# Kernel tuning notes

Measured on AMD Instinct MI355X. Metric: run time of the kernel, lower is better.

Reference implementation:

```python
import jax, jax.numpy as jnp
import numpy as np

B, M, N, P, Q, GRID, DIM = 8, 64, 64, 3, 3, 512, 3


def _clamped_knots(n_ctrl, p):
    # clamped uniform knot vector of length n_ctrl + p + 1
    interior = np.linspace(0.0, 1.0, n_ctrl - p + 1)[1:-1]
    return np.concatenate([np.zeros(p + 1), interior, np.ones(p + 1)]).astype(np.float32)


def _find_span(u, knots, n_ctrl, p):
    spans = np.searchsorted(knots, u, side='right') - 1
    return np.clip(spans, p, n_ctrl - 1).astype(np.int32)


def _basis_funs(u, spans, knots, p):
    # Cox-de Boor (Algorithm A2.2, The NURBS Book), vectorized over the grid
    G = u.shape[0]
    Nb = np.zeros((G, p + 1), np.float32)
    Nb[:, 0] = 1.0
    left = np.zeros((G, p + 1), np.float32)
    right = np.zeros((G, p + 1), np.float32)
    for j in range(1, p + 1):
        left[:, j] = u - knots[spans + 1 - j]
        right[:, j] = knots[spans + j] - u
        saved = np.zeros(G, np.float32)
        for r in range(j):
            temp = Nb[:, r] / (right[:, r + 1] + left[:, j - r])
            Nb[:, r] = saved + right[:, r + 1] * temp
            saved = left[:, j - r] * temp
        Nb[:, j] = saved
    return Nb


def setup_inputs() -> dict:
    key = jax.random.key(0)
    k1, k2 = jax.random.split(key)
    U = _clamped_knots(M, P)
    V = _clamped_knots(N, Q)
    u = np.linspace(0.0, 1.0, GRID, dtype=np.float32)
    v = np.linspace(0.0, 1.0, GRID, dtype=np.float32)
    uspan = _find_span(u, U, M, P)
    vspan = _find_span(v, V, N, Q)
    Nu = _basis_funs(u, uspan, U, P)
    Nv = _basis_funs(v, vspan, V, Q)
    xyz = jax.random.normal(k1, (B, M, N, DIM), jnp.float32)
    w = jax.random.uniform(k2, (B, M, N, 1), jnp.float32, minval=0.5, maxval=1.5)
    ctrl_pts = jnp.concatenate([xyz * w, w], axis=-1)  # homogeneous [B,M,N,4]
    return {
        'ctrl_pts': ctrl_pts,
        'uspan': jnp.asarray(uspan),
        'vspan': jnp.asarray(vspan),
        'Nu': jnp.asarray(Nu),
        'Nv': jnp.asarray(Nv),
    }


def reference(ctrl_pts, uspan, vspan, Nu, Nv):
    # surfaces[b,i,j,:] = sum_{r,s} Nu[i,r] Nv[j,s] ctrl[b, uspan[i]-P+r, vspan[j]-Q+s, :]
    idx_u = uspan[:, None] - P + jnp.arange(P + 1)   # [G, P+1]
    idx_v = vspan[:, None] - Q + jnp.arange(Q + 1)   # [G, Q+1]
    pts_u = ctrl_pts[:, idx_u]                        # [B, G, P+1, N, 4] gather
    Su = jnp.einsum('gr,bgrnd->bgnd', Nu, pts_u)      # [B, G, N, 4]
    pts_v = Su[:, :, idx_v]                           # [B, G, G, Q+1, 4] gather
    Sw = jnp.einsum('hs,bghsd->bghd', Nv, pts_v)      # [B, G, G, 4] homogeneous
    return Sw[..., :DIM] / Sw[..., DIM:DIM + 1]       # perspective divide
```

## Files before the change

### kernel.cpp

```cpp
#include <hip/hip_runtime.h>

#define GRID_PTS 512
#define M_CTRL   64
#define N_CTRL   64

__global__ __launch_bounds__(128) void surfeval_kernel(
    const float4* __restrict__ ctrl,
    const int*    __restrict__ uspan,
    const int*    __restrict__ vspan,
    const float4* __restrict__ Nu,
    const float4* __restrict__ Nv,
    float*        __restrict__ out)
{
    __shared__ float4 Su[N_CTRL];

    const int blk = blockIdx.x;
    const int g   = blk & (GRID_PTS - 1);
    const int b   = blk >> 9;
    const int t   = threadIdx.x;

    if (t < N_CTRL) {
        const int    iu = uspan[g] - 3;
        const float4 nu = Nu[g];
        const float4* cp = ctrl + ((size_t)b * M_CTRL + iu) * N_CTRL + t;
        const float4 c0 = cp[0 * N_CTRL];
        const float4 c1 = cp[1 * N_CTRL];
        const float4 c2 = cp[2 * N_CTRL];
        const float4 c3 = cp[3 * N_CTRL];
        float4 s;
        s.x = nu.x * c0.x + nu.y * c1.x + nu.z * c2.x + nu.w * c3.x;
        s.y = nu.x * c0.y + nu.y * c1.y + nu.z * c2.y + nu.w * c3.y;
        s.z = nu.x * c0.z + nu.y * c1.z + nu.z * c2.z + nu.w * c3.z;
        s.w = nu.x * c0.w + nu.y * c1.w + nu.z * c2.w + nu.w * c3.w;
        Su[t] = s;
    }
    __syncthreads();

    const int h0 = t * 4;
    float r[12];
#pragma unroll
    for (int i = 0; i < 4; ++i) {
        const int    h  = h0 + i;
        const int    iv = vspan[h] - 3;
        const float4 nv = Nv[h];
        const float4 a0 = Su[iv + 0];
        const float4 a1 = Su[iv + 1];
        const float4 a2 = Su[iv + 2];
        const float4 a3 = Su[iv + 3];
        const float sx = nv.x * a0.x + nv.y * a1.x + nv.z * a2.x + nv.w * a3.x;
        const float sy = nv.x * a0.y + nv.y * a1.y + nv.z * a2.y + nv.w * a3.y;
        const float sz = nv.x * a0.z + nv.y * a1.z + nv.z * a2.z + nv.w * a3.z;
        const float sw = nv.x * a0.w + nv.y * a1.w + nv.z * a2.w + nv.w * a3.w;
        const float inv = 1.0f / sw;
        r[i * 3 + 0] = sx * inv;
        r[i * 3 + 1] = sy * inv;
        r[i * 3 + 2] = sz * inv;
    }

    float4* op = (float4*)(out + ((size_t)blk * GRID_PTS + h0) * 3);
    op[0] = make_float4(r[0], r[1], r[2],  r[3]);
    op[1] = make_float4(r[4], r[5], r[6],  r[7]);
    op[2] = make_float4(r[8], r[9], r[10], r[11]);
}

extern "C" void kernel_launch(void* const* d_in, const int* in_sizes, int n_in,
                              void* d_out, int out_size, void* d_ws, size_t ws_size,
                              hipStream_t stream) {
    const float4* ctrl  = (const float4*)d_in[0];
    const int*    uspan = (const int*)d_in[1];
    const int*    vspan = (const int*)d_in[2];
    const float4* Nu    = (const float4*)d_in[3];
    const float4* Nv    = (const float4*)d_in[4];
    float*        out   = (float*)d_out;

    const int blocks = 8 * GRID_PTS;
    surfeval_kernel<<<blocks, 128, 0, stream>>>(ctrl, uspan, vspan, Nu, Nv, out);
}
```

Baseline: 75.66 us.

## Hoist Nv/vspan loads before barrier, use fast rcp and nontemporal stores

Moves each thread's vspan and Nv loads ahead of the Su computation and barrier so their latency overlaps with the first stage. It replaces the IEEE division with the hardware reciprocal builtin and writes the output with nontemporal vector stores to avoid polluting cache. The output writes dominate traffic, so the nontemporal stores target write bandwidth. The fast reciprocal slightly reduces precision.

```diff
diff --git a/kernel.cpp b/kernel.cpp
--- a/kernel.cpp
+++ b/kernel.cpp
@@ -3,6 +3,8 @@
 #define GRID_PTS 512
 #define M_CTRL   64
 #define N_CTRL   64
+
+typedef float vfloat4 __attribute__((ext_vector_type(4)));
 
 __global__ __launch_bounds__(128) void surfeval_kernel(
     const float4* __restrict__ ctrl,
@@ -18,6 +20,15 @@
     const int g   = blk & (GRID_PTS - 1);
     const int b   = blk >> 9;
     const int t   = threadIdx.x;
+    const int h0  = t * 4;
+
+    int    iv[4];
+    float4 nv[4];
+#pragma unroll
+    for (int i = 0; i < 4; ++i) {
+        iv[i] = vspan[h0 + i] - 3;
+        nv[i] = Nv[h0 + i];
+    }
 
     if (t < N_CTRL) {
         const int    iu = uspan[g] - 3;
@@ -36,31 +47,31 @@
     }
     __syncthreads();
 
-    const int h0 = t * 4;
     float r[12];
 #pragma unroll
     for (int i = 0; i < 4; ++i) {
-        const int    h  = h0 + i;
-        const int    iv = vspan[h] - 3;
-        const float4 nv = Nv[h];
-        const float4 a0 = Su[iv + 0];
-        const float4 a1 = Su[iv + 1];
-        const float4 a2 = Su[iv + 2];
-        const float4 a3 = Su[iv + 3];
-        const float sx = nv.x * a0.x + nv.y * a1.x + nv.z * a2.x + nv.w * a3.x;
-        const float sy = nv.x * a0.y + nv.y * a1.y + nv.z * a2.y + nv.w * a3.y;
-        const float sz = nv.x * a0.z + nv.y * a1.z + nv.z * a2.z + nv.w * a3.z;
-        const float sw = nv.x * a0.w + nv.y * a1.w + nv.z * a2.w + nv.w * a3.w;
-        const float inv = 1.0f / sw;
+        const float4 a0 = Su[iv[i] + 0];
+        const float4 a1 = Su[iv[i] + 1];
+        const float4 a2 = Su[iv[i] + 2];
+        const float4 a3 = Su[iv[i] + 3];
+        const float4 n  = nv[i];
+        const float sx = n.x * a0.x + n.y * a1.x + n.z * a2.x + n.w * a3.x;
+        const float sy = n.x * a0.y + n.y * a1.y + n.z * a2.y + n.w * a3.y;
+        const float sz = n.x * a0.z + n.y * a1.z + n.z * a2.z + n.w * a3.z;
+        const float sw = n.x * a0.w + n.y * a1.w + n.z * a2.w + n.w * a3.w;
+        const float inv = __builtin_amdgcn_rcpf(sw);
         r[i * 3 + 0] = sx * inv;
         r[i * 3 + 1] = sy * inv;
         r[i * 3 + 2] = sz * inv;
     }
 
-    float4* op = (float4*)(out + ((size_t)blk * GRID_PTS + h0) * 3);
-    op[0] = make_float4(r[0], r[1], r[2],  r[3]);
-    op[1] = make_float4(r[4], r[5], r[6],  r[7]);
-    op[2] = make_float4(r[8], r[9], r[10], r[11]);
+    vfloat4* op = (vfloat4*)(out + ((size_t)blk * GRID_PTS + h0) * 3);
+    vfloat4 o0 = { r[0], r[1], r[2],  r[3]  };
+    vfloat4 o1 = { r[4], r[5], r[6],  r[7]  };
+    vfloat4 o2 = { r[8], r[9], r[10], r[11] };
+    __builtin_nontemporal_store(o0, op + 0);
+    __builtin_nontemporal_store(o1, op + 1);
+    __builtin_nontemporal_store(o2, op + 2);
 }
 
 extern "C" void kernel_launch(void* const* d_in, const int* in_sizes, int n_in,
```

After: 76.00 us. Within noise of the previous version (+0.4%).
